# Kernel tuning notes

Measured on AMD Instinct MI355X. Metric: run time of the kernel, lower is better.

Reference implementation:

```python
import jax, jax.numpy as jnp
import numpy as np

LATENT_DIM = 64
HIDDEN = 2 * LATENT_DIM
MAX_STEPS = 100
DT = 0.05
DAMPING = 0.01
PERT_SCALE = 1e-4
EPS = 1e-8


def setup_inputs() -> dict:
    key = jax.random.key(0)
    ks = jax.random.split(key, 9)
    B = 2048
    initial_state = 0.05 * jax.random.normal(ks[0], (B, LATENT_DIM), dtype=jnp.float32)
    pd = jax.random.normal(ks[1], (B, LATENT_DIM), dtype=jnp.float32)
    pd = pd / (jnp.linalg.norm(pd, axis=-1, keepdims=True) + EPS)
    def lin(k, fan_in, shape):
        bound = 1.0 / np.sqrt(fan_in)
        return jax.random.uniform(k, shape, jnp.float32, -bound, bound)
    W1 = lin(ks[2], LATENT_DIM, (LATENT_DIM, HIDDEN)); b1 = lin(ks[3], LATENT_DIM, (HIDDEN,))
    W2 = lin(ks[4], HIDDEN, (HIDDEN, LATENT_DIM)); b2 = lin(ks[5], HIDDEN, (LATENT_DIM,))
    W3 = lin(ks[6], LATENT_DIM, (LATENT_DIM, 1)); b3 = lin(ks[7], LATENT_DIM, (1,))
    return {"initial_state": initial_state, "perturbation_direction": pd,
            "W1": W1, "b1": b1, "W2": W2, "b2": b2, "W3": W3, "b3": b3}


def _potential(q, W1, b1, W2, b2, W3, b3):
    h = jax.nn.silu(q @ W1 + b1)
    h = jax.nn.silu(h @ W2 + b2)
    return (h @ W3 + b3)[..., 0]  # [B]


def _mobius_add(x, y):
    x2 = jnp.sum(x * x, axis=-1, keepdims=True)
    y2 = jnp.sum(y * y, axis=-1, keepdims=True)
    xy = jnp.sum(x * y, axis=-1, keepdims=True)
    num = (1 + 2 * xy + y2) * x + (1 - x2) * y
    den = 1 + 2 * xy + x2 * y2
    r = num / (den + EPS)
    rn = jnp.linalg.norm(r, axis=-1, keepdims=True)
    return jnp.where(rn > 0.99, r * 0.99 / (rn + EPS), r)


def _exp_map(x, v):
    vn = jnp.linalg.norm(v, axis=-1, keepdims=True) + EPS
    x2 = jnp.minimum(jnp.sum(x * x, axis=-1, keepdims=True), 0.999)
    lam = 2.0 / (1 - x2)
    mag = jnp.tanh(jnp.minimum(lam * vn / 2, 15.0))
    return _mobius_add(x, mag * (v / vn))


def _hyp_dist(x, y):
    d2 = jnp.sum((x - y) ** 2, axis=-1)
    x2 = jnp.minimum(jnp.sum(x * x, axis=-1), 0.999)
    y2 = jnp.minimum(jnp.sum(y * y, axis=-1), 0.999)
    arg = 1 + 2 * d2 / ((1 - x2) * (1 - y2) + EPS)
    return jnp.arccosh(jnp.maximum(arg, 1.0 + EPS))


def _leapfrog(q, p, params):
    gradV = jax.grad(lambda qq: jnp.sum(_potential(qq, *params)))(q)
    p_half = (p - 0.5 * DT * gradV) * (1 - DAMPING)
    q2 = jnp.minimum(jnp.sum(q * q, axis=-1, keepdims=True), 0.999)
    lam = 2.0 / (1 - q2)
    q_new = _exp_map(q, DT * (p_half / lam ** 2))
    gradV_new = jax.grad(lambda qq: jnp.sum(_potential(qq, *params)))(q_new)
    p_new = p_half - 0.5 * DT * gradV_new
    return q_new, p_new


def reference(initial_state, perturbation_direction, W1, b1, W2, b2, W3, b3):
    params = (W1, b1, W2, b2, W3, b3)
    q0 = initial_state
    q_pert = initial_state + PERT_SCALE * perturbation_direction
    qpn = jnp.linalg.norm(q_pert, axis=-1, keepdims=True)
    q_pert = jnp.where(qpn > 0.99, q_pert * 0.99 / (qpn + EPS), q_pert)
    p0 = jnp.zeros_like(q0)
    p_pert = jnp.zeros_like(q_pert)

    def step(carry, _):
        q0, p0, qp, pp = carry
        d = _hyp_dist(q0, qp)  # [B]
        q0, p0 = _leapfrog(q0, p0, params)
        qp, pp = _leapfrog(qp, pp, params)
        return (q0, p0, qp, pp), d

    _, distances = jax.lax.scan(step, (q0, p0, q_pert, p_pert), None, length=MAX_STEPS)
    return distances  # [MAX_STEPS, B]
```

## Files before the change

### kernel.cpp

```cpp
#include <hip/hip_runtime.h>
#include <math.h>

namespace {

constexpr int   STEPS = 100;
constexpr int   BATCH = 2048;
constexpr float DT    = 0.05f;
constexpr float DAMP  = 0.01f;
constexpr float EPSV  = 1e-8f;
constexpr int   NT    = 2;

__device__ __forceinline__ float wsum(float v) {
#pragma unroll
  for (int o = 32; o > 0; o >>= 1) v += __shfl_xor(v, o, 64);
  return v;
}

__global__ __launch_bounds__(256, 2)
void geo_scramble_kernel(const float* __restrict__ q0g, const float* __restrict__ pdg,
                         const float* __restrict__ W1g, const float* __restrict__ b1g,
                         const float* __restrict__ W2g, const float* __restrict__ b2g,
                         const float* __restrict__ W3g, float* __restrict__ out)
{
  __shared__ __align__(16) float W1s[64 * 130];
  __shared__ __align__(16) float W2Ts[64 * 130];
  __shared__ __align__(16) float stg_all[4][NT][128];

  const int tid  = threadIdx.x;
  const int lane = tid & 63;
  const int wave = tid >> 6;

  for (int idx = tid; idx < 64 * 128; idx += 256) {
    int r = idx >> 7, c = idx & 127;
    W1s[r * 130 + c] = W1g[idx];
  }
  for (int idx = tid; idx < 64 * 128; idx += 256) {
    int j = idx >> 7, k = idx & 127;
    W2Ts[j * 130 + k] = W2g[k * 64 + j];
  }
  __syncthreads();

  const float rb10 = b1g[2 * lane];
  const float rb11 = b1g[2 * lane + 1];
  const float rb2  = b2g[lane];
  const float rw3  = W3g[lane];

  float (*stg)[128] = stg_all[wave];
  const int pair = blockIdx.x * 4 + wave;
  const int l2 = lane << 1;

  float q[NT], p[NT], g[NT];
#pragma unroll
  for (int t = 0; t < NT; ++t) {
    float base = q0g[pair * 64 + lane];
    if (t & 1) {
      float qp = base + 1e-4f * pdg[pair * 64 + lane];
      float n  = sqrtf(wsum(qp * qp));
      float sc = (n > 0.99f) ? (0.99f / (n + EPSV)) : 1.0f;
      q[t] = qp * sc;
    } else {
      q[t] = base;
    }
    p[t] = 0.0f;
  }

  auto evalgrad = [&](const float* x, float* gr) {
#pragma unroll
    for (int t = 0; t < NT; ++t) stg[t][lane] = x[t];

    float a0[NT], a1[NT];
#pragma unroll
    for (int t = 0; t < NT; ++t) { a0[t] = rb10; a1[t] = rb11; }
    for (int i = 0; i < 64; i += 4) {
      float bq[NT][4];
#pragma unroll
      for (int t = 0; t < NT; ++t) {
        float4 v = *(const float4*)&stg[t][i];
        bq[t][0] = v.x; bq[t][1] = v.y; bq[t][2] = v.z; bq[t][3] = v.w;
      }
#pragma unroll
      for (int u = 0; u < 4; ++u) {
        float2 w = *(const float2*)&W1s[(i + u) * 130 + l2];
#pragma unroll
        for (int t = 0; t < NT; ++t) {
          a0[t] = fmaf(bq[t][u], w.x, a0[t]);
          a1[t] = fmaf(bq[t][u], w.y, a1[t]);
        }
      }
    }

    float d10[NT], d11[NT];
#pragma unroll
    for (int t = 0; t < NT; ++t) {
      float z  = a0[t];
      float s  = 1.0f / (1.0f + expf(-z));
      float h0 = z * s;
      d10[t]   = s * (1.0f + z * (1.0f - s));
      float zb = a1[t];
      float sb = 1.0f / (1.0f + expf(-zb));
      float h1 = zb * sb;
      d11[t]   = sb * (1.0f + zb * (1.0f - sb));
      float2 hh; hh.x = h0; hh.y = h1;
      *(float2*)&stg[t][l2] = hh;
    }

    float a2[NT];
#pragma unroll
    for (int t = 0; t < NT; ++t) a2[t] = rb2;
    for (int k = 0; k < 128; k += 4) {
      float bh[NT][4];
#pragma unroll
      for (int t = 0; t < NT; ++t) {
        float4 v = *(const float4*)&stg[t][k];
        bh[t][0] = v.x; bh[t][1] = v.y; bh[t][2] = v.z; bh[t][3] = v.w;
      }
      float2 wA = *(const float2*)&W2Ts[lane * 130 + k];
      float2 wB = *(const float2*)&W2Ts[lane * 130 + k + 2];
#pragma unroll
      for (int t = 0; t < NT; ++t) {
        a2[t] = fmaf(bh[t][0], wA.x, a2[t]);
        a2[t] = fmaf(bh[t][1], wA.y, a2[t]);
        a2[t] = fmaf(bh[t][2], wB.x, a2[t]);
        a2[t] = fmaf(bh[t][3], wB.y, a2[t]);
      }
    }

#pragma unroll
    for (int t = 0; t < NT; ++t) {
      float z = a2[t];
      float s = 1.0f / (1.0f + expf(-z));
      stg[t][lane] = rw3 * (s * (1.0f + z * (1.0f - s)));
    }

    float c0[NT], c1[NT];
#pragma unroll
    for (int t = 0; t < NT; ++t) { c0[t] = 0.0f; c1[t] = 0.0f; }
    for (int j = 0; j < 64; j += 4) {
      float bg[NT][4];
#pragma unroll
      for (int t = 0; t < NT; ++t) {
        float4 v = *(const float4*)&stg[t][j];
        bg[t][0] = v.x; bg[t][1] = v.y; bg[t][2] = v.z; bg[t][3] = v.w;
      }
#pragma unroll
      for (int u = 0; u < 4; ++u) {
        float2 w = *(const float2*)&W2Ts[(j + u) * 130 + l2];
#pragma unroll
        for (int t = 0; t < NT; ++t) {
          c0[t] = fmaf(bg[t][u], w.x, c0[t]);
          c1[t] = fmaf(bg[t][u], w.y, c1[t]);
        }
      }
    }

#pragma unroll
    for (int t = 0; t < NT; ++t) {
      float2 gg; gg.x = c0[t] * d10[t]; gg.y = c1[t] * d11[t];
      *(float2*)&stg[t][l2] = gg;
    }

#pragma unroll
    for (int t = 0; t < NT; ++t) gr[t] = 0.0f;
    for (int k = 0; k < 128; k += 4) {
      float bg[NT][4];
#pragma unroll
      for (int t = 0; t < NT; ++t) {
        float4 v = *(const float4*)&stg[t][k];
        bg[t][0] = v.x; bg[t][1] = v.y; bg[t][2] = v.z; bg[t][3] = v.w;
      }
      float2 wA = *(const float2*)&W1s[lane * 130 + k];
      float2 wB = *(const float2*)&W1s[lane * 130 + k + 2];
#pragma unroll
      for (int t = 0; t < NT; ++t) {
        gr[t] = fmaf(bg[t][0], wA.x, gr[t]);
        gr[t] = fmaf(bg[t][1], wA.y, gr[t]);
        gr[t] = fmaf(bg[t][2], wB.x, gr[t]);
        gr[t] = fmaf(bg[t][3], wB.y, gr[t]);
      }
    }
  };

  evalgrad(q, g);

  for (int s = 0; s < STEPS; ++s) {
    {
      float xq = q[0], yq = q[1];
      float df = xq - yq;
      float d2 = wsum(df * df);
      float x2 = fminf(wsum(xq * xq), 0.999f);
      float y2 = fminf(wsum(yq * yq), 0.999f);
      float arg = 1.0f + 2.0f * d2 / ((1.0f - x2) * (1.0f - y2) + EPSV);
      float d = acoshf(fmaxf(arg, 1.0f + EPSV));
      if (lane == 0) out[s * BATCH + pair] = d;
    }

    float qn[NT], ph[NT];
#pragma unroll
    for (int t = 0; t < NT; ++t) {
      ph[t] = (p[t] - 0.5f * DT * g[t]) * (1.0f - DAMP);
      float q2r = wsum(q[t] * q[t]);
      float q2c = fminf(q2r, 0.999f);
      float lam = 2.0f / (1.0f - q2c);
      float v   = DT * ph[t] / (lam * lam);
      float vn  = sqrtf(wsum(v * v)) + EPSV;
      float mag = tanhf(fminf(lam * vn * 0.5f, 15.0f));
      float y   = mag * (v / vn);
      float y2  = wsum(y * y);
      float xy  = wsum(q[t] * y);
      float num = (1.0f + 2.0f * xy + y2) * q[t] + (1.0f - q2r) * y;
      float den = 1.0f + 2.0f * xy + q2r * y2;
      float r   = num / (den + EPSV);
      float rn  = sqrtf(wsum(r * r));
      float sc  = (rn > 0.99f) ? (0.99f / (rn + EPSV)) : 1.0f;
      qn[t] = r * sc;
    }

    evalgrad(qn, g);
#pragma unroll
    for (int t = 0; t < NT; ++t) {
      p[t] = ph[t] - 0.5f * DT * g[t];
      q[t] = qn[t];
    }
  }
}

}

extern "C" void kernel_launch(void* const* d_in, const int* in_sizes, int n_in,
                              void* d_out, int out_size, void* d_ws, size_t ws_size,
                              hipStream_t stream) {
  (void)in_sizes; (void)n_in; (void)out_size; (void)d_ws; (void)ws_size;
  const float* q0 = (const float*)d_in[0];
  const float* pd = (const float*)d_in[1];
  const float* W1 = (const float*)d_in[2];
  const float* b1 = (const float*)d_in[3];
  const float* W2 = (const float*)d_in[4];
  const float* b2 = (const float*)d_in[5];
  const float* W3 = (const float*)d_in[6];
  float* out = (float*)d_out;

  geo_scramble_kernel<<<dim3(512), dim3(256), 0, stream>>>(q0, pd, W1, b1, W2, b2, W3, out);
}
```

Baseline: 986.9 us.

## Read W1 and W2 directly from global memory instead of shared copies

Drops the shared-memory copy of W1 and reads W1 and W2 weights straight from global memory (through the cache) in two of the four matvecs, using float4 loads where the layout allows. Adds unroll pragmas, widens the W2T shared reads to float4, and reuses the per-step squared-norm reductions instead of recomputing them. The goal is lower LDS traffic and footprint, possibly allowing higher occupancy. The cost is that global/L1 loads with strided per-lane addresses (e.g. W2g[l2*64+j], W1g[lane*128+k]) add latency and may coalesce poorly.

```diff
diff --git a/kernel.cpp b/kernel.cpp
--- a/kernel.cpp
+++ b/kernel.cpp
@@ -9,6 +9,7 @@
 constexpr float DAMP  = 0.01f;
 constexpr float EPSV  = 1e-8f;
 constexpr int   NT    = 2;
+constexpr int   LDW   = 130;
 
 __device__ __forceinline__ float wsum(float v) {
 #pragma unroll
@@ -22,8 +23,7 @@
                          const float* __restrict__ W2g, const float* __restrict__ b2g,
                          const float* __restrict__ W3g, float* __restrict__ out)
 {
-  __shared__ __align__(16) float W1s[64 * 130];
-  __shared__ __align__(16) float W2Ts[64 * 130];
+  __shared__ __align__(16) float W2Ts[64 * LDW];
   __shared__ __align__(16) float stg_all[4][NT][128];
 
   const int tid  = threadIdx.x;
@@ -31,12 +31,8 @@
   const int wave = tid >> 6;
 
   for (int idx = tid; idx < 64 * 128; idx += 256) {
-    int r = idx >> 7, c = idx & 127;
-    W1s[r * 130 + c] = W1g[idx];
-  }
-  for (int idx = tid; idx < 64 * 128; idx += 256) {
     int j = idx >> 7, k = idx & 127;
-    W2Ts[j * 130 + k] = W2g[k * 64 + j];
+    W2Ts[j * LDW + k] = W2g[k * 64 + j];
   }
   __syncthreads();
 
@@ -71,6 +67,7 @@
     float a0[NT], a1[NT];
 #pragma unroll
     for (int t = 0; t < NT; ++t) { a0[t] = rb10; a1[t] = rb11; }
+#pragma unroll 4
     for (int i = 0; i < 64; i += 4) {
       float bq[NT][4];
 #pragma unroll
@@ -80,7 +77,7 @@
       }
 #pragma unroll
       for (int u = 0; u < 4; ++u) {
-        float2 w = *(const float2*)&W1s[(i + u) * 130 + l2];
+        float2 w = *(const float2*)&W1g[(i + u) * 128 + l2];
 #pragma unroll
         for (int t = 0; t < NT; ++t) {
           a0[t] = fmaf(bq[t][u], w.x, a0[t]);
@@ -107,6 +104,7 @@
     float a2[NT];
 #pragma unroll
     for (int t = 0; t < NT; ++t) a2[t] = rb2;
+#pragma unroll 8
     for (int k = 0; k < 128; k += 4) {
       float bh[NT][4];
 #pragma unroll
@@ -114,14 +112,13 @@
         float4 v = *(const float4*)&stg[t][k];
         bh[t][0] = v.x; bh[t][1] = v.y; bh[t][2] = v.z; bh[t][3] = v.w;
       }
-      float2 wA = *(const float2*)&W2Ts[lane * 130 + k];
-      float2 wB = *(const float2*)&W2Ts[lane * 130 + k + 2];
-#pragma unroll
-      for (int t = 0; t < NT; ++t) {
-        a2[t] = fmaf(bh[t][0], wA.x, a2[t]);
-        a2[t] = fmaf(bh[t][1], wA.y, a2[t]);
-        a2[t] = fmaf(bh[t][2], wB.x, a2[t]);
-        a2[t] = fmaf(bh[t][3], wB.y, a2[t]);
+      float4 w = *(const float4*)&W2Ts[lane * LDW + k];
+#pragma unroll
+      for (int t = 0; t < NT; ++t) {
+        a2[t] = fmaf(bh[t][0], w.x, a2[t]);
+        a2[t] = fmaf(bh[t][1], w.y, a2[t]);
+        a2[t] = fmaf(bh[t][2], w.z, a2[t]);
+        a2[t] = fmaf(bh[t][3], w.w, a2[t]);
       }
     }
 
@@ -135,6 +132,7 @@
     float c0[NT], c1[NT];
 #pragma unroll
     for (int t = 0; t < NT; ++t) { c0[t] = 0.0f; c1[t] = 0.0f; }
+#pragma unroll 4
     for (int j = 0; j < 64; j += 4) {
       float bg[NT][4];
 #pragma unroll
@@ -142,14 +140,23 @@
         float4 v = *(const float4*)&stg[t][j];
         bg[t][0] = v.x; bg[t][1] = v.y; bg[t][2] = v.z; bg[t][3] = v.w;
       }
-#pragma unroll
-      for (int u = 0; u < 4; ++u) {
-        float2 w = *(const float2*)&W2Ts[(j + u) * 130 + l2];
-#pragma unroll
-        for (int t = 0; t < NT; ++t) {
-          c0[t] = fmaf(bg[t][u], w.x, c0[t]);
-          c1[t] = fmaf(bg[t][u], w.y, c1[t]);
-        }
+      float4 wxA = *(const float4*)&W2g[l2 * 64 + j];
+      float4 wxB = *(const float4*)&W2g[(l2 + 1) * 64 + j];
+#pragma unroll
+      for (int t = 0; t < NT; ++t) {
+        c0[t] = fmaf(bg[t][0], wxA.x, c0[t]); c1[t] = fmaf(bg[t][0], wxB.x, c1[t]);
+      }
+#pragma unroll
+      for (int t = 0; t < NT; ++t) {
+        c0[t] = fmaf(bg[t][1], wxA.y, c0[t]); c1[t] = fmaf(bg[t][1], wxB.y, c1[t]);
+      }
+#pragma unroll
+      for (int t = 0; t < NT; ++t) {
+        c0[t] = fmaf(bg[t][2], wxA.z, c0[t]); c1[t] = fmaf(bg[t][2], wxB.z, c1[t]);
+      }
+#pragma unroll
+      for (int t = 0; t < NT; ++t) {
+        c0[t] = fmaf(bg[t][3], wxA.w, c0[t]); c1[t] = fmaf(bg[t][3], wxB.w, c1[t]);
       }
     }
 
@@ -161,6 +168,7 @@
 
 #pragma unroll
     for (int t = 0; t < NT; ++t) gr[t] = 0.0f;
+#pragma unroll 8
     for (int k = 0; k < 128; k += 4) {
       float bg[NT][4];
 #pragma unroll
@@ -168,14 +176,13 @@
         float4 v = *(const float4*)&stg[t][k];
         bg[t][0] = v.x; bg[t][1] = v.y; bg[t][2] = v.z; bg[t][3] = v.w;
       }
-      float2 wA = *(const float2*)&W1s[lane * 130 + k];
-      float2 wB = *(const float2*)&W1s[lane * 130 + k + 2];
-#pragma unroll
-      for (int t = 0; t < NT; ++t) {
-        gr[t] = fmaf(bg[t][0], wA.x, gr[t]);
-        gr[t] = fmaf(bg[t][1], wA.y, gr[t]);
-        gr[t] = fmaf(bg[t][2], wB.x, gr[t]);
-        gr[t] = fmaf(bg[t][3], wB.y, gr[t]);
+      float4 w = *(const float4*)&W1g[lane * 128 + k];
+#pragma unroll
+      for (int t = 0; t < NT; ++t) {
+        gr[t] = fmaf(bg[t][0], w.x, gr[t]);
+        gr[t] = fmaf(bg[t][1], w.y, gr[t]);
+        gr[t] = fmaf(bg[t][2], w.z, gr[t]);
+        gr[t] = fmaf(bg[t][3], w.w, gr[t]);
       }
     }
   };
@@ -183,12 +190,14 @@
   evalgrad(q, g);
 
   for (int s = 0; s < STEPS; ++s) {
+    float qq0 = wsum(q[0] * q[0]);
+    float qq1 = wsum(q[1] * q[1]);
+
     {
-      float xq = q[0], yq = q[1];
-      float df = xq - yq;
+      float df = q[0] - q[1];
       float d2 = wsum(df * df);
-      float x2 = fminf(wsum(xq * xq), 0.999f);
-      float y2 = fminf(wsum(yq * yq), 0.999f);
+      float x2 = fminf(qq0, 0.999f);
+      float y2 = fminf(qq1, 0.999f);
       float arg = 1.0f + 2.0f * d2 / ((1.0f - x2) * (1.0f - y2) + EPSV);
       float d = acoshf(fmaxf(arg, 1.0f + EPSV));
       if (lane == 0) out[s * BATCH + pair] = d;
@@ -198,7 +207,7 @@
 #pragma unroll
     for (int t = 0; t < NT; ++t) {
       ph[t] = (p[t] - 0.5f * DT * g[t]) * (1.0f - DAMP);
-      float q2r = wsum(q[t] * q[t]);
+      float q2r = (t == 0) ? qq0 : qq1;
       float q2c = fminf(q2r, 0.999f);
       float lam = 2.0f / (1.0f - q2c);
       float v   = DT * ph[t] / (lam * lam);
```

After: 1.807 ms. +83.1%, slower.
